# Performance work log

Hardware: AMD Instinct MI355X
Metric: run time of the kernel (lower is better)

Reference implementation:

```python
import jax, jax.numpy as jnp
import numpy as np

H, W = 16, 64
HK, WK = 7, 11
NUM_HEADS = 8
DIM = 512
HEAD_DIM = DIM // NUM_HEADS
SCALE = HEAD_DIM ** -0.5
N = H * W


def _local_mask():
    # Additive mask [N, N]: 0 inside the local window, -inf outside.
    # Equivalent to the torch loop: token (h,w) attends to (i,j) with
    # |i-h| <= HK//2 and |j-w| <= WK//2 (odd kernel, centered crop).
    h = jnp.arange(H)
    w = jnp.arange(W)
    hh, ww = jnp.meshgrid(h, w, indexing='ij')  # [H, W]
    q_h = hh.reshape(-1)  # [N]
    q_w = ww.reshape(-1)
    in_win = (jnp.abs(q_h[:, None] - q_h[None, :]) <= HK // 2) & \
             (jnp.abs(q_w[:, None] - q_w[None, :]) <= WK // 2)
    return jnp.where(in_win, 0.0, -jnp.inf).astype(jnp.float32)  # [N, N]


def setup_inputs() -> dict:
    key = jax.random.key(0)
    k1, k2, k3 = jax.random.split(key, 3)
    x = jax.random.normal(k1, (64, N, DIM), dtype=jnp.float32)
    w_qkv = jax.random.normal(k2, (DIM, 3 * DIM), dtype=jnp.float32) * 0.02
    w_proj = jax.random.normal(k3, (DIM, DIM), dtype=jnp.float32) * 0.02
    b_proj = jnp.zeros((DIM,), dtype=jnp.float32)
    return {"x": x, "w_qkv": w_qkv, "w_proj": w_proj, "b_proj": b_proj}


def reference(x, w_qkv, w_proj, b_proj):
    B = x.shape[0]
    mask = _local_mask()  # [N, N]
    qkv = (x @ w_qkv).reshape(B, N, 3, NUM_HEADS, HEAD_DIM)
    q = qkv[:, :, 0].transpose(0, 2, 1, 3) * SCALE  # [B, h, N, d]
    k = qkv[:, :, 1].transpose(0, 2, 1, 3)
    v = qkv[:, :, 2].transpose(0, 2, 1, 3)
    attn = jnp.einsum('bhnd,bhmd->bhnm', q, k) + mask  # [B, h, N, N]
    attn = jax.nn.softmax(attn, axis=-1)
    out = jnp.einsum('bhnm,bhmd->bhnd', attn, v)
    out = out.transpose(0, 2, 1, 3).reshape(B, N, DIM)
    return out @ w_proj + b_proj
```

## Files before the change

kernel.cpp:

```cpp
#include <hip/hip_runtime.h>
#include <hip/hip_bf16.h>
#include <stdint.h>

#define HGRID   16
#define WGRID   64
#define NTOK    1024
#define BATCH   64
#define NHEADS  8
#define HDIM    64
#define DMODEL  512
#define BH_TOT  512
#define QK_SCALE (0.125f * 1.44269504089f)

typedef __attribute__((ext_vector_type(8))) short short8;
typedef __attribute__((ext_vector_type(4))) float floatx4;

__device__ __forceinline__ short f2bf(float f) {
    union { float f; uint32_t u; } c{f};
    uint32_t r = (c.u + 0x7fffu + ((c.u >> 16) & 1u)) >> 16;
    return (short)r;
}

__device__ __forceinline__ void gload_lds16(const void* g, void* l) {
    auto gp = (const __attribute__((address_space(1))) void*)(uintptr_t)g;
    auto lp = (__attribute__((address_space(3))) void*)(uint32_t)(uintptr_t)l;
    __builtin_amdgcn_global_load_lds(gp, lp, 16, 0, 0);
}

__global__ __launch_bounds__(256)
void cast_x_kernel(const float* __restrict__ in, short* __restrict__ out) {
    size_t i = (size_t)blockIdx.x * 256 + threadIdx.x;
    const float4* in4 = (const float4*)in;
    float4 a = in4[i * 2];
    float4 b = in4[i * 2 + 1];
    short8 o;
    o[0] = f2bf(a.x); o[1] = f2bf(a.y); o[2] = f2bf(a.z); o[3] = f2bf(a.w);
    o[4] = f2bf(b.x); o[5] = f2bf(b.y); o[6] = f2bf(b.z); o[7] = f2bf(b.w);
    *(short8*)(out + i * 8) = o;
}

__global__ __launch_bounds__(256)
void tcast_kernel(const float* __restrict__ in, short* __restrict__ out, int R, int C) {
    __shared__ short tile[64][72];
    int r0 = blockIdx.x * 64, c0 = blockIdx.y * 64;
    int t = threadIdx.x;
#pragma unroll
    for (int i = 0; i < 16; i++) {
        int s = i * 256 + t;
        int r = s >> 6, c = s & 63;
        tile[r][c] = f2bf(in[(size_t)(r0 + r) * C + c0 + c]);
    }
    __syncthreads();
#pragma unroll
    for (int i = 0; i < 16; i++) {
        int s = i * 256 + t;
        int c = s >> 6, r = s & 63;
        out[(size_t)(c0 + c) * R + r0 + r] = tile[r][c];
    }
}

template <int MODE>
__global__ __launch_bounds__(256)
void gemm_kernel(const short* __restrict__ A, const short* __restrict__ Bm,
                 short* __restrict__ qo, short* __restrict__ ko, short* __restrict__ vo,
                 float* __restrict__ outf, const float* __restrict__ bias) {
    __shared__ short As[128 * 32];
    __shared__ short Bs[128 * 32];
    const int bn = blockIdx.x, bm = blockIdx.y;
    const int t = threadIdx.x;
    const int w = t >> 6;
    const int l = t & 63;
    const int wm = w >> 1, wn = w & 1;
    const int lq = l & 15, quad = l >> 4;

    const floatx4 zero = {0.f, 0.f, 0.f, 0.f};
    floatx4 acc[4][4];
#pragma unroll
    for (int i = 0; i < 4; i++)
#pragma unroll
        for (int j = 0; j < 4; j++) acc[i][j] = zero;

    const short* Ab = A + (size_t)bm * 128 * 512;
    const short* Bb = Bm + (size_t)bn * 128 * 512;

    for (int k0 = 0; k0 < 512; k0 += 32) {
        __syncthreads();
#pragma unroll
        for (int i = 0; i < 2; i++) {
            int s = i * 256 + t;
            int r = s >> 2, c8 = (s & 3) * 8;
            gload_lds16(Ab + (size_t)r * 512 + k0 + c8, &As[s * 8]);
            gload_lds16(Bb + (size_t)r * 512 + k0 + c8, &Bs[s * 8]);
        }
        __syncthreads();

        short8 af[4], bfr[4];
#pragma unroll
        for (int mi = 0; mi < 4; mi++)
            af[mi] = *(const short8*)&As[(wm * 64 + mi * 16 + lq) * 32 + quad * 8];
#pragma unroll
        for (int ni = 0; ni < 4; ni++)
            bfr[ni] = *(const short8*)&Bs[(wn * 64 + ni * 16 + lq) * 32 + quad * 8];
#pragma unroll
        for (int mi = 0; mi < 4; mi++)
#pragma unroll
            for (int ni = 0; ni < 4; ni++)
                acc[mi][ni] = __builtin_amdgcn_mfma_f32_16x16x32_bf16(
                    af[mi], bfr[ni], acc[mi][ni], 0, 0, 0);
    }

#pragma unroll
    for (int mi = 0; mi < 4; mi++)
#pragma unroll
        for (int ni = 0; ni < 4; ni++)
#pragma unroll
            for (int r = 0; r < 4; r++) {
                int row = bm * 128 + wm * 64 + mi * 16 + quad * 4 + r;
                int col = bn * 128 + wn * 64 + ni * 16 + lq;
                float val = acc[mi][ni][r];
                if (MODE == 0) {
                    int bidx = row >> 10, tok = row & 1023;
                    int which = col >> 9, hd = (col >> 6) & 7, dd = col & 63;
                    size_t didx = (((size_t)bidx * NHEADS + hd) * NTOK + tok) * HDIM + dd;
                    if (which == 0)       qo[didx] = f2bf(val * QK_SCALE);
                    else if (which == 1)  ko[didx] = f2bf(val);
                    else                  vo[didx] = f2bf(val);
                } else {
                    outf[(size_t)row * DMODEL + col] = val + bias[col];
                }
            }
}

__global__ __launch_bounds__(256)
void tv_kernel(const short* __restrict__ v, short* __restrict__ vT) {
    __shared__ short tile[64][72];
    int tt = blockIdx.x;
    int bh = blockIdx.y;
    int t = threadIdx.x;
    const short* src = v + ((size_t)bh * NTOK + tt * 64) * HDIM;
#pragma unroll
    for (int i = 0; i < 2; i++) {
        int s = i * 256 + t;
        int r = s >> 3, c8 = (s & 7) * 8;
        *(short8*)&tile[r][c8] = *(const short8*)(src + r * HDIM + c8);
    }
    __syncthreads();
    short* dst = vT + (size_t)bh * HDIM * NTOK + tt * 64;
#pragma unroll
    for (int i = 0; i < 2; i++) {
        int s = i * 256 + t;
        int d = s & 63, t0 = (s >> 6) * 8;
        short8 g;
#pragma unroll
        for (int j = 0; j < 8; j++) g[j] = tile[t0 + j][d];
        *(short8*)(dst + (size_t)d * NTOK + t0) = g;
    }
}

__global__ __launch_bounds__(256)
void attn_kernel(const short* __restrict__ q, const short* __restrict__ k,
                 const short* __restrict__ vT, short* __restrict__ ao) {
    const int bid = blockIdx.x;
    const int h = (bid >> 3) & 15;
    const int bh = (bid & 7) + 8 * (bid >> 7);
    const int b = bh >> 3, head = bh & 7;
    const int t = threadIdx.x;
    const int w = t >> 6;
    const int l = t & 63;
    const int lq = l & 15, quad = l >> 4;

    __shared__ short Kc[64][72];
    __shared__ short Vc[80][72];
    __shared__ short Pc[4][16][40];

    const int s_w = (w == 0) ? 0 : (w == 1) ? 8 : (w == 2) ? 24 : 32;

    const short* qbp = q + ((size_t)bh * NTOK + h * 64 + w * 16 + lq) * HDIM + quad * 8;
    short8 qa0 = *(const short8*)(qbp);
    short8 qa1 = *(const short8*)(qbp + 32);

    bool ok[2][4];
#pragma unroll
    for (int nt = 0; nt < 2; nt++)
#pragma unroll
        for (int r = 0; r < 4; r++) {
            int kw_g = s_w + nt * 16 + lq;
            int qi = w * 16 + quad * 4 + r;
            int dw = kw_g - qi;
            ok[nt][r] = (dw <= 5) && (dw >= -5);
        }

    const floatx4 zero = {0.f, 0.f, 0.f, 0.f};
    floatx4 O[5];
#pragma unroll
    for (int i = 0; i < 5; i++) O[i] = zero;

    if (t < 64) Vc[64][t] = (short)0x3F80;

    const int kh0 = (h - 3 < 0) ? 0 : h - 3;
    const int kh1 = (h + 3 > HGRID - 1) ? HGRID - 1 : h + 3;

    for (int kh = kh0; kh <= kh1; ++kh) {
        __syncthreads();
        {
            const short* kb = k + ((size_t)bh * NTOK + kh * 64) * HDIM;
            const short* vb = vT + (size_t)bh * HDIM * NTOK + kh * 64;
#pragma unroll
            for (int i = 0; i < 2; i++) {
                int s = i * 256 + t;
                int r = s >> 3, c8 = (s & 7) * 8;
                *(short8*)&Kc[r][c8] = *(const short8*)(kb + r * HDIM + c8);
                *(short8*)&Vc[r][c8] = *(const short8*)(vb + (size_t)r * NTOK + c8);
            }
        }
        __syncthreads();

        floatx4 S[2];
#pragma unroll
        for (int nt = 0; nt < 2; nt++) {
            S[nt] = zero;
            short8 b0 = *(const short8*)&Kc[s_w + nt * 16 + lq][quad * 8];
            short8 b1 = *(const short8*)&Kc[s_w + nt * 16 + lq][quad * 8 + 32];
            S[nt] = __builtin_amdgcn_mfma_f32_16x16x32_bf16(qa0, b0, S[nt], 0, 0, 0);
            S[nt] = __builtin_amdgcn_mfma_f32_16x16x32_bf16(qa1, b1, S[nt], 0, 0, 0);
        }

#pragma unroll
        for (int nt = 0; nt < 2; nt++)
#pragma unroll
            for (int r = 0; r < 4; r++) {
                float p = ok[nt][r] ? exp2f(S[nt][r]) : 0.f;
                Pc[w][quad * 4 + r][nt * 16 + lq] = f2bf(p);
            }

        short8 pa = *(const short8*)&Pc[w][lq][quad * 8];
#pragma unroll
        for (int dt = 0; dt < 5; dt++) {
            short8 vf = *(const short8*)&Vc[dt * 16 + lq][s_w + quad * 8];
            O[dt] = __builtin_amdgcn_mfma_f32_16x16x32_bf16(pa, vf, O[dt], 0, 0, 0);
        }
    }

    float inv[4];
#pragma unroll
    for (int r = 0; r < 4; r++) {
        float s = __shfl(O[4][r], l & 48);
        inv[r] = 1.0f / s;
    }

#pragma unroll
    for (int dt = 0; dt < 4; dt++)
#pragma unroll
        for (int r = 0; r < 4; r++) {
            int qi = w * 16 + quad * 4 + r;
            int d = dt * 16 + lq;
            float o = O[dt][r] * inv[r];
            ao[((size_t)b * NTOK + h * 64 + qi) * DMODEL + head * HDIM + d] = f2bf(o);
        }
}

extern "C" void kernel_launch(void* const* d_in, const int* in_sizes, int n_in,
                              void* d_out, int out_size, void* d_ws, size_t ws_size,
                              hipStream_t stream) {
    const float* x      = (const float*)d_in[0];
    const float* w_qkv  = (const float*)d_in[1];
    const float* w_proj = (const float*)d_in[2];
    const float* b_proj = (const float*)d_in[3];
    float* out = (float*)d_out;

    const size_t SZ_X    = (size_t)BATCH * NTOK * DMODEL * 2;
    const size_t SZ_HEAD = (size_t)BH_TOT * NTOK * HDIM * 2;
    char* p = (char*)d_ws;
    short* xb     = (short*)p; p += SZ_X;
    short* wqkvT  = (short*)p; p += (size_t)1536 * 512 * 2;
    short* wprojT = (short*)p; p += (size_t)512 * 512 * 2;
    short* qb     = (short*)p; p += SZ_HEAD;
    short* kb     = (short*)p; p += SZ_HEAD;
    short* vb     = (short*)p; p += SZ_HEAD;
    short* vTb    = (short*)p; p += SZ_HEAD;
    short* ao     = xb;

    cast_x_kernel<<<dim3((BATCH * NTOK * DMODEL) / (256 * 8)), dim3(256), 0, stream>>>(x, xb);
    tcast_kernel<<<dim3(512 / 64, 1536 / 64), dim3(256), 0, stream>>>(w_qkv, wqkvT, 512, 1536);
    tcast_kernel<<<dim3(512 / 64, 512 / 64), dim3(256), 0, stream>>>(w_proj, wprojT, 512, 512);
    gemm_kernel<0><<<dim3(1536 / 128, 65536 / 128), dim3(256), 0, stream>>>(
        xb, wqkvT, qb, kb, vb, nullptr, nullptr);
    tv_kernel<<<dim3(NTOK / 64, BH_TOT), dim3(256), 0, stream>>>(vb, vTb);
    attn_kernel<<<dim3(HGRID * BH_TOT), dim3(256), 0, stream>>>(qb, kb, vTb, ao);
    gemm_kernel<1><<<dim3(512 / 128, 65536 / 128), dim3(256), 0, stream>>>(
        ao, wprojT, nullptr, nullptr, nullptr, out, b_proj);
}
```

Baseline: 565.8 us.

## Remap GEMM blocks per XCD, double K-tile, and use k-major LDS layout

```diff
diff --git a/kernel.cpp b/kernel.cpp
--- a/kernel.cpp
+++ b/kernel.cpp
@@ -59,14 +59,18 @@
     }
 }
 
-template <int MODE>
+template <int MODE, int NBN>
 __global__ __launch_bounds__(256)
 void gemm_kernel(const short* __restrict__ A, const short* __restrict__ Bm,
                  short* __restrict__ qo, short* __restrict__ ko, short* __restrict__ vo,
                  float* __restrict__ outf, const float* __restrict__ bias) {
-    __shared__ short As[128 * 32];
-    __shared__ short Bs[128 * 32];
-    const int bn = blockIdx.x, bm = blockIdx.y;
+    __shared__ __align__(16) short As[8][128][8];
+    __shared__ __align__(16) short Bs[8][128][8];
+    const int bid = blockIdx.x;
+    const int xcd = bid & 7;
+    const int jj = bid >> 3;
+    const int bm = xcd * 64 + jj / NBN;
+    const int bn = jj % NBN;
     const int t = threadIdx.x;
     const int w = t >> 6;
     const int l = t & 63;
@@ -82,31 +86,36 @@
 
     const short* Ab = A + (size_t)bm * 128 * 512;
     const short* Bb = Bm + (size_t)bn * 128 * 512;
-
-    for (int k0 = 0; k0 < 512; k0 += 32) {
+    short* As0 = &As[0][0][0];
+    short* Bs0 = &Bs[0][0][0];
+
+    for (int k0 = 0; k0 < 512; k0 += 64) {
         __syncthreads();
 #pragma unroll
-        for (int i = 0; i < 2; i++) {
+        for (int i = 0; i < 4; i++) {
             int s = i * 256 + t;
-            int r = s >> 2, c8 = (s & 3) * 8;
-            gload_lds16(Ab + (size_t)r * 512 + k0 + c8, &As[s * 8]);
-            gload_lds16(Bb + (size_t)r * 512 + k0 + c8, &Bs[s * 8]);
+            int kc = s >> 7, r = s & 127;
+            gload_lds16(Ab + (size_t)r * 512 + k0 + kc * 8, As0 + s * 8);
+            gload_lds16(Bb + (size_t)r * 512 + k0 + kc * 8, Bs0 + s * 8);
         }
         __syncthreads();
 
-        short8 af[4], bfr[4];
-#pragma unroll
-        for (int mi = 0; mi < 4; mi++)
-            af[mi] = *(const short8*)&As[(wm * 64 + mi * 16 + lq) * 32 + quad * 8];
-#pragma unroll
-        for (int ni = 0; ni < 4; ni++)
-            bfr[ni] = *(const short8*)&Bs[(wn * 64 + ni * 16 + lq) * 32 + quad * 8];
-#pragma unroll
-        for (int mi = 0; mi < 4; mi++)
+#pragma unroll
+        for (int ks = 0; ks < 2; ks++) {
+            short8 af[4], bfr[4];
+#pragma unroll
+            for (int mi = 0; mi < 4; mi++)
+                af[mi] = *(const short8*)&As[4 * ks + quad][wm * 64 + mi * 16 + lq][0];
 #pragma unroll
             for (int ni = 0; ni < 4; ni++)
-                acc[mi][ni] = __builtin_amdgcn_mfma_f32_16x16x32_bf16(
-                    af[mi], bfr[ni], acc[mi][ni], 0, 0, 0);
+                bfr[ni] = *(const short8*)&Bs[4 * ks + quad][wn * 64 + ni * 16 + lq][0];
+#pragma unroll
+            for (int mi = 0; mi < 4; mi++)
+#pragma unroll
+                for (int ni = 0; ni < 4; ni++)
+                    acc[mi][ni] = __builtin_amdgcn_mfma_f32_16x16x32_bf16(
+                        af[mi], bfr[ni], acc[mi][ni], 0, 0, 0);
+        }
     }
 
 #pragma unroll
@@ -283,10 +292,10 @@
     cast_x_kernel<<<dim3((BATCH * NTOK * DMODEL) / (256 * 8)), dim3(256), 0, stream>>>(x, xb);
     tcast_kernel<<<dim3(512 / 64, 1536 / 64), dim3(256), 0, stream>>>(w_qkv, wqkvT, 512, 1536);
     tcast_kernel<<<dim3(512 / 64, 512 / 64), dim3(256), 0, stream>>>(w_proj, wprojT, 512, 512);
-    gemm_kernel<0><<<dim3(1536 / 128, 65536 / 128), dim3(256), 0, stream>>>(
+    gemm_kernel<0, 12><<<dim3(8 * 64 * 12), dim3(256), 0, stream>>>(
         xb, wqkvT, qb, kb, vb, nullptr, nullptr);
     tv_kernel<<<dim3(NTOK / 64, BH_TOT), dim3(256), 0, stream>>>(vb, vTb);
     attn_kernel<<<dim3(HGRID * BH_TOT), dim3(256), 0, stream>>>(qb, kb, vTb, ao);
-    gemm_kernel<1><<<dim3(512 / 128, 65536 / 128), dim3(256), 0, stream>>>(
+    gemm_kernel<1, 4><<<dim3(8 * 64 * 4), dim3(256), 0, stream>>>(
         ao, wprojT, nullptr, nullptr, nullptr, out, b_proj);
 }
```

After: 703.1 us. 1.24x slower.
